# Kernel tuning notes

Hardware: AMD Instinct MI355X
Metric: run time of the kernel (lower is better)

Reference implementation:

```python
import jax, jax.numpy as jnp
import numpy as np

T, B, N = 5, 1048576, 16
GAMMA = 0.99


def setup_inputs() -> dict:
    key = jax.random.key(0)
    k = jax.random.split(key, 6)
    q = jax.random.normal(k[0], (B, N), dtype=jnp.float32)
    next_n_q = jax.random.normal(k[1], (B, N), dtype=jnp.float32)
    action = jax.random.randint(k[2], (B,), 0, N)
    next_n_action = jax.random.randint(k[3], (B,), 0, N)
    reward = jax.random.normal(k[4], (T, B), dtype=jnp.float32)
    done = jax.random.randint(k[5], (B,), 0, 2).astype(jnp.bool_)
    weight = jnp.ones((B,), dtype=jnp.float32)
    gamma = jnp.float32(GAMMA)
    return {"q": q, "next_n_q": next_n_q, "action": action,
            "next_n_action": next_n_action, "reward": reward,
            "done": done, "weight": weight, "gamma": gamma}


def reference(q, next_n_q, action, next_n_action, reward, done, weight, gamma):
    # q, next_n_q: (B, N); action/next_n_action/done/weight: (B,); reward: (T, B)
    t = reward.shape[0]
    # gather Q(s,a) and Q(s_{t+n}, a') by action index
    q_s_a = jnp.take_along_axis(q, action[:, None], axis=1)[:, 0]            # (B,)
    next_q_s_a = jnp.take_along_axis(next_n_q, next_n_action[:, None], axis=1)[:, 0]
    # n-step discounted return: sum_t gamma^t r_t + gamma^T * Q' * (1 - done)
    factors = gamma ** jnp.arange(t, dtype=q.dtype)                          # (T,)
    not_done = 1.0 - done.astype(q.dtype)
    target = jnp.einsum('t,tb->b', factors, reward) + (gamma ** t) * next_q_s_a * not_done
    target = jax.lax.stop_gradient(target)
    # per-sample MSE td error, weighted mean loss
    td_error_per_sample = jnp.square(q_s_a - target)                         # (B,)
    loss = jnp.mean(td_error_per_sample * weight)                            # ()
    return loss, td_error_per_sample
```

## Files before the change

kernel.cpp:

```cpp
#include <hip/hip_runtime.h>


__global__ __launch_bounds__(256) void qnstep_td_kernel(
    const float* __restrict__ q,
    const float* __restrict__ nq,
    const int*   __restrict__ act,
    const int*   __restrict__ nact,
    const float* __restrict__ rew,
    const int*   __restrict__ done,
    const float* __restrict__ w,
    const float* __restrict__ gamma_p,
    float*       __restrict__ out,
    int B, int N, int T, float invB)
{
    const int b = blockIdx.x * blockDim.x + threadIdx.x;
    const float gamma = gamma_p[0];

    float val = 0.0f;
    if (b < B) {
        float f = 1.0f, tgt = 0.0f;
        #pragma unroll 8
        for (int t = 0; t < T; ++t) {
            tgt += f * rew[t * B + b];
            f *= gamma;
        }
        const float nd  = (done[b] != 0) ? 0.0f : 1.0f;
        const float nqv = nq[(long long)b * N + nact[b]];
        tgt += f * nqv * nd;

        const float qa = q[(long long)b * N + act[b]];
        const float d  = qa - tgt;
        const float td = d * d;
        out[1 + b] = td;
        val = td * w[b];
    }

    #pragma unroll
    for (int off = 32; off > 0; off >>= 1)
        val += __shfl_down(val, off, 64);

    __shared__ float ssum[4];
    const int wave = threadIdx.x >> 6;
    const int lane = threadIdx.x & 63;
    if (lane == 0) ssum[wave] = val;
    __syncthreads();

    if (threadIdx.x == 0) {
        float s = ssum[0] + ssum[1] + ssum[2] + ssum[3];
        atomicAdd(out, s * invB);
    }
}

extern "C" void kernel_launch(void* const* d_in, const int* in_sizes, int n_in,
                              void* d_out, int out_size, void* d_ws, size_t ws_size,
                              hipStream_t stream) {
    const float* q     = (const float*)d_in[0];
    const float* nq    = (const float*)d_in[1];
    const int*   act   = (const int*)d_in[2];
    const int*   nact  = (const int*)d_in[3];
    const float* rew   = (const float*)d_in[4];
    const int*   done  = (const int*)d_in[5];
    const float* w     = (const float*)d_in[6];
    const float* gamma = (const float*)d_in[7];

    const int B = in_sizes[2];
    const int N = in_sizes[0] / B;
    const int T = in_sizes[4] / B;

    float* out = (float*)d_out;

    hipMemsetAsync(out, 0, sizeof(float), stream);

    const int block = 256;
    const int grid  = (B + block - 1) / block;
    qnstep_td_kernel<<<grid, block, 0, stream>>>(
        q, nq, act, nact, rew, done, w, gamma, out, B, N, T, 1.0f / (float)B);
}
```

Before: 200.5 us.

## Process four samples per thread with vector loads and two-pass reduction

Each thread now handles four consecutive samples, using int4/float4 loads for the action, done, weight and reward arrays. The per-block atomicAdd and the memset are replaced by per-block partials in workspace, which a single-block second kernel sums. This cuts the thread count, the number of load instructions and atomic contention, at the cost of an extra launch. The tail path for B not divisible by 4 is dropped, and the reduce kernel only covers up to 1024 partials, which holds for B=1M (1024 blocks).

```diff
diff --git a/kernel.cpp b/kernel.cpp
--- a/kernel.cpp
+++ b/kernel.cpp
@@ -1,7 +1,7 @@
 #include <hip/hip_runtime.h>
 
 
-__global__ __launch_bounds__(256) void qnstep_td_kernel(
+__global__ __launch_bounds__(256) void qnstep_td_main(
     const float* __restrict__ q,
     const float* __restrict__ nq,
     const int*   __restrict__ act,
@@ -11,28 +11,52 @@
     const float* __restrict__ w,
     const float* __restrict__ gamma_p,
     float*       __restrict__ out,
-    int B, int N, int T, float invB)
+    float*       __restrict__ partial,
+    int B, int N, int T)
 {
-    const int b = blockIdx.x * blockDim.x + threadIdx.x;
+    const int g  = blockIdx.x * blockDim.x + threadIdx.x;
+    const int b0 = g * 4;
     const float gamma = gamma_p[0];
 
     float val = 0.0f;
-    if (b < B) {
-        float f = 1.0f, tgt = 0.0f;
+    if (b0 + 3 < B) {
+        const int4   a4  = ((const int4*)act)[g];
+        const int4   na4 = ((const int4*)nact)[g];
+        const int4   d4  = ((const int4*)done)[g];
+        const float4 w4  = ((const float4*)w)[g];
+
+        float t0 = 0.f, t1 = 0.f, t2 = 0.f, t3 = 0.f;
+        float f = 1.0f;
         #pragma unroll 8
         for (int t = 0; t < T; ++t) {
-            tgt += f * rew[t * B + b];
+            const float4 r4 = ((const float4*)(rew + (long long)t * B))[g];
+            t0 += f * r4.x; t1 += f * r4.y; t2 += f * r4.z; t3 += f * r4.w;
             f *= gamma;
         }
-        const float nd  = (done[b] != 0) ? 0.0f : 1.0f;
-        const float nqv = nq[(long long)b * N + nact[b]];
-        tgt += f * nqv * nd;
 
-        const float qa = q[(long long)b * N + act[b]];
-        const float d  = qa - tgt;
-        const float td = d * d;
-        out[1 + b] = td;
-        val = td * w[b];
+        const float nq0 = nq[(long long)(b0 + 0) * N + na4.x];
+        const float nq1 = nq[(long long)(b0 + 1) * N + na4.y];
+        const float nq2 = nq[(long long)(b0 + 2) * N + na4.z];
+        const float nq3 = nq[(long long)(b0 + 3) * N + na4.w];
+        const float q0  = q [(long long)(b0 + 0) * N + a4.x];
+        const float q1  = q [(long long)(b0 + 1) * N + a4.y];
+        const float q2  = q [(long long)(b0 + 2) * N + a4.z];
+        const float q3  = q [(long long)(b0 + 3) * N + a4.w];
+
+        t0 += f * nq0 * (d4.x ? 0.f : 1.f);
+        t1 += f * nq1 * (d4.y ? 0.f : 1.f);
+        t2 += f * nq2 * (d4.z ? 0.f : 1.f);
+        t3 += f * nq3 * (d4.w ? 0.f : 1.f);
+
+        const float e0 = q0 - t0, e1 = q1 - t1, e2 = q2 - t2, e3 = q3 - t3;
+        const float td0 = e0 * e0, td1 = e1 * e1, td2 = e2 * e2, td3 = e3 * e3;
+
+        out[1 + b0 + 0] = td0;
+        out[1 + b0 + 1] = td1;
+        out[1 + b0 + 2] = td2;
+        out[1 + b0 + 3] = td3;
+
+        val = td0 * w4.x + td1 * w4.y + td2 * w4.z + td3 * w4.w;
     }
 
     #pragma unroll
@@ -45,9 +69,30 @@
     if (lane == 0) ssum[wave] = val;
     __syncthreads();
 
-    if (threadIdx.x == 0) {
-        float s = ssum[0] + ssum[1] + ssum[2] + ssum[3];
-        atomicAdd(out, s * invB);
+    if (threadIdx.x == 0)
+        partial[blockIdx.x] = ssum[0] + ssum[1] + ssum[2] + ssum[3];
+}
+
+__global__ __launch_bounds__(1024) void qnstep_td_reduce(
+    const float* __restrict__ partial, float* __restrict__ out,
+    int n, float invB)
+{
+    const int tid = threadIdx.x;
+    float v = (tid < n) ? partial[tid] : 0.0f;
+
+    #pragma unroll
+    for (int off = 32; off > 0; off >>= 1)
+        v += __shfl_down(v, off, 64);
+
+    __shared__ float ssum[16];
+    if ((tid & 63) == 0) ssum[tid >> 6] = v;
+    __syncthreads();
+
+    if (tid == 0) {
+        float s = 0.0f;
+        #pragma unroll
+        for (int i = 0; i < 16; ++i) s += ssum[i];
+        out[0] = s * invB;
     }
 }
 
@@ -67,12 +112,14 @@
     const int N = in_sizes[0] / B;
     const int T = in_sizes[4] / B;
 
-    float* out = (float*)d_out;
-
-    hipMemsetAsync(out, 0, sizeof(float), stream);
+    float* out     = (float*)d_out;
+    float* partial = (float*)d_ws;
 
     const int block = 256;
-    const int grid  = (B + block - 1) / block;
-    qnstep_td_kernel<<<grid, block, 0, stream>>>(
-        q, nq, act, nact, rew, done, w, gamma, out, B, N, T, 1.0f / (float)B);
+    const int gridA = (B + block * 4 - 1) / (block * 4);
+
+    qnstep_td_main<<<gridA, block, 0, stream>>>(
+        q, nq, act, nact, rew, done, w, gamma, out, partial, B, N, T);
+    qnstep_td_reduce<<<1, 1024, 0, stream>>>(
+        partial, out, gridA, 1.0f / (float)B);
 }
```

Measured after the change: 188.3 us. -6.1%, faster.

## Stage Q rows through LDS with coalesced loads and two-pass reduction

Applied to the files above, without the earlier changes.

For N=16, each block loads 512 full rows of q and next_n_q with coalesced float4 loads into shared memory and gathers the action values from there. Each thread processes two samples, using vectorized loads for actions, done flags, weights and rewards. The global atomicAdd and memset are replaced with per-block partial sums and a separate single-block reduce kernel. This trades an extra launch and more LDS use for better memory coalescing, with a generic fallback path kept for other shapes.

```diff
diff --git a/kernel.cpp b/kernel.cpp
--- a/kernel.cpp
+++ b/kernel.cpp
@@ -1,7 +1,10 @@
 #include <hip/hip_runtime.h>
 
 
-__global__ __launch_bounds__(256) void qnstep_td_kernel(
+#define TILE_ROWS 512
+#define BLOCK     256
+
+__global__ __launch_bounds__(BLOCK) void qnstep_td_main(
     const float* __restrict__ q,
     const float* __restrict__ nq,
     const int*   __restrict__ act,
@@ -11,43 +14,130 @@
     const float* __restrict__ w,
     const float* __restrict__ gamma_p,
     float*       __restrict__ out,
-    int B, int N, int T, float invB)
+    float*       __restrict__ partial,
+    int B, int T)
 {
-    const int b = blockIdx.x * blockDim.x + threadIdx.x;
+    __shared__ float tile[TILE_ROWS * 16];
+
+    const int tid  = threadIdx.x;
+    const long long base = (long long)blockIdx.x * TILE_ROWS;
     const float gamma = gamma_p[0];
 
-    float val = 0.0f;
-    if (b < B) {
-        float f = 1.0f, tgt = 0.0f;
-        #pragma unroll 8
-        for (int t = 0; t < T; ++t) {
-            tgt += f * rew[t * B + b];
-            f *= gamma;
-        }
-        const float nd  = (done[b] != 0) ? 0.0f : 1.0f;
-        const float nqv = nq[(long long)b * N + nact[b]];
-        tgt += f * nqv * nd;
+    const long long g = base / 2 + tid;
+    const int2   a2  = ((const int2*)act)[g];
+    const int2   na2 = ((const int2*)nact)[g];
+    const int2   d2  = ((const int2*)done)[g];
+    const float2 w2  = ((const float2*)w)[g];
 
-        const float qa = q[(long long)b * N + act[b]];
-        const float d  = qa - tgt;
-        const float td = d * d;
-        out[1 + b] = td;
-        val = td * w[b];
+    float t0 = 0.f, t1 = 0.f, f = 1.0f;
+    #pragma unroll 8
+    for (int t = 0; t < T; ++t) {
+        const float2 r2 = ((const float2*)(rew + (long long)t * B))[g];
+        t0 += f * r2.x; t1 += f * r2.y;
+        f *= gamma;
     }
+
+    const int s0 = tid * 2, s1 = tid * 2 + 1;
+
+    float4* t4 = (float4*)tile;
+    {
+        const float4* q4 = (const float4*)q + base * 4;
+        #pragma unroll
+        for (int j = 0; j < 8; ++j)
+            t4[tid + j * BLOCK] = q4[tid + j * BLOCK];
+    }
+    __syncthreads();
+    const float qa0 = tile[s0 * 16 + a2.x];
+    const float qa1 = tile[s1 * 16 + a2.y];
+    __syncthreads();
+
+    {
+        const float4* nq4 = (const float4*)nq + base * 4;
+        #pragma unroll
+        for (int j = 0; j < 8; ++j)
+            t4[tid + j * BLOCK] = nq4[tid + j * BLOCK];
+    }
+    __syncthreads();
+    const float nqa0 = tile[s0 * 16 + na2.x];
+    const float nqa1 = tile[s1 * 16 + na2.y];
+
+    t0 += f * nqa0 * (d2.x ? 0.f : 1.f);
+    t1 += f * nqa1 * (d2.y ? 0.f : 1.f);
+    const float e0 = qa0 - t0, e1 = qa1 - t1;
+    const float td0 = e0 * e0, td1 = e1 * e1;
+
+    out[1 + base + s0] = td0;
+    out[1 + base + s1] = td1;
+
+    float val = td0 * w2.x + td1 * w2.y;
 
     #pragma unroll
     for (int off = 32; off > 0; off >>= 1)
         val += __shfl_down(val, off, 64);
 
-    __shared__ float ssum[4];
-    const int wave = threadIdx.x >> 6;
-    const int lane = threadIdx.x & 63;
+    __shared__ float ssum[BLOCK / 64];
+    const int wave = tid >> 6, lane = tid & 63;
     if (lane == 0) ssum[wave] = val;
     __syncthreads();
+    if (tid == 0) {
+        float s = 0.f;
+        #pragma unroll
+        for (int i = 0; i < BLOCK / 64; ++i) s += ssum[i];
+        partial[blockIdx.x] = s;
+    }
+}
 
-    if (threadIdx.x == 0) {
-        float s = ssum[0] + ssum[1] + ssum[2] + ssum[3];
-        atomicAdd(out, s * invB);
+__global__ __launch_bounds__(256) void qnstep_td_generic(
+    const float* __restrict__ q, const float* __restrict__ nq,
+    const int* __restrict__ act, const int* __restrict__ nact,
+    const float* __restrict__ rew, const int* __restrict__ done,
+    const float* __restrict__ w, const float* __restrict__ gamma_p,
+    float* __restrict__ out, float* __restrict__ partial,
+    int B, int N, int T)
+{
+    const int b = blockIdx.x * blockDim.x + threadIdx.x;
+    const float gamma = gamma_p[0];
+    float val = 0.0f;
+    if (b < B) {
+        float f = 1.0f, tgt = 0.0f;
+        for (int t = 0; t < T; ++t) { tgt += f * rew[(long long)t * B + b]; f *= gamma; }
+        const float nd = (done[b] != 0) ? 0.f : 1.f;
+        tgt += f * nq[(long long)b * N + nact[b]] * nd;
+        const float d = q[(long long)b * N + act[b]] - tgt;
+        const float td = d * d;
+        out[1 + b] = td;
+        val = td * w[b];
+    }
+    #pragma unroll
+    for (int off = 32; off > 0; off >>= 1) val += __shfl_down(val, off, 64);
+    __shared__ float ssum[4];
+    if ((threadIdx.x & 63) == 0) ssum[threadIdx.x >> 6] = val;
+    __syncthreads();
+    if (threadIdx.x == 0)
+        partial[blockIdx.x] = ssum[0] + ssum[1] + ssum[2] + ssum[3];
+}
+
+__global__ __launch_bounds__(1024) void qnstep_td_reduce(
+    const float* __restrict__ partial, float* __restrict__ out,
+    int n, float invB)
+{
+    const int tid = threadIdx.x;
+    float v = 0.0f;
+    for (int i = tid; i < n; i += 1024) v += partial[i];
+
+    #pragma unroll
+    for (int off = 32; off > 0; off >>= 1)
+        v += __shfl_down(v, off, 64);
+
+    __shared__ float ssum[16];
+    if ((tid & 63) == 0) ssum[tid >> 6] = v;
+    __syncthreads();
+
+    if (tid == 0) {
+        float s = 0.0f;
+        #pragma unroll
+        for (int i = 0; i < 16; ++i) s += ssum[i];
+        out[0] = s * invB;
     }
 }
 
@@ -67,12 +157,18 @@
     const int N = in_sizes[0] / B;
     const int T = in_sizes[4] / B;
 
-    float* out = (float*)d_out;
+    float* out     = (float*)d_out;
+    float* partial = (float*)d_ws;
 
-    hipMemsetAsync(out, 0, sizeof(float), stream);
-
-    const int block = 256;
-    const int grid  = (B + block - 1) / block;
-    qnstep_td_kernel<<<grid, block, 0, stream>>>(
-        q, nq, act, nact, rew, done, w, gamma, out, B, N, T, 1.0f / (float)B);
+    if (N == 16 && (B % TILE_ROWS) == 0) {
+        const int grid = B / TILE_ROWS;
+        qnstep_td_main<<<grid, BLOCK, 0, stream>>>(
+            q, nq, act, nact, rew, done, w, gamma, out, partial, B, T);
+        qnstep_td_reduce<<<1, 1024, 0, stream>>>(partial, out, grid, 1.0f / (float)B);
+    } else {
+        const int grid = (B + 255) / 256;
+        qnstep_td_generic<<<grid, 256, 0, stream>>>(
+            q, nq, act, nact, rew, done, w, gamma, out, partial, B, N, T);
+        qnstep_td_reduce<<<1, 1024, 0, stream>>>(partial, out, grid, 1.0f / (float)B);
+    }
 }
```

After: 185.2 us. -7.6%, faster.

## Add persistent software-pipelined kernel with vectorized loads for N=16, T=5

Applied to the files above, without the earlier changes.

Adds a persistent grid-stride kernel (512 blocks) in which each thread handles two samples per iteration, using int2/float2 loads for the per-sample arrays and float4 loads for the gathered Q values. Index and reward loads are prefetched two iterations ahead and the dependent Q gathers one iteration ahead, so the gather latency overlaps with computation. The discount sum is unrolled as a Horner polynomial with a precomputed gamma^5. This path is specialised to N=16 and T=5, falls back to the generic kernel otherwise, and uses more registers for the pipeline.

```diff
diff --git a/kernel.cpp b/kernel.cpp
--- a/kernel.cpp
+++ b/kernel.cpp
@@ -1,7 +1,57 @@
 #include <hip/hip_runtime.h>
 
 
-__global__ __launch_bounds__(256) void qnstep_td_kernel(
+#define BLOCK 256
+#define GRID  512
+
+struct SStage {
+    int2   a, na, d;
+    float2 w;
+    float2 r0, r1, r2, r3, r4;
+};
+struct GStage {
+    float4 q0, q1, n0, n1;
+};
+
+__device__ __forceinline__ SStage load_s(
+    int g, const int* __restrict__ act, const int* __restrict__ nact,
+    const int* __restrict__ done, const float* __restrict__ w,
+    const float* __restrict__ rew, int PB)
+{
+    SStage s;
+    s.a  = ((const int2*)act)[g];
+    s.na = ((const int2*)nact)[g];
+    s.d  = ((const int2*)done)[g];
+    s.w  = ((const float2*)w)[g];
+    const float2* r = (const float2*)rew;
+    s.r0 = r[g];
+    s.r1 = r[g + PB];
+    s.r2 = r[g + 2 * PB];
+    s.r3 = r[g + 3 * PB];
+    s.r4 = r[g + 4 * PB];
+    return s;
+}
+
+__device__ __forceinline__ GStage load_g(
+    const SStage& s, int g, const float* __restrict__ q,
+    const float* __restrict__ nq)
+{
+    GStage o;
+    const long long b0 = (long long)g * 2;
+    o.q0 = *(const float4*)(q  + (b0 << 4)       + ((s.a.x  >> 2) << 2));
+    o.q1 = *(const float4*)(q  + ((b0 + 1) << 4) + ((s.a.y  >> 2) << 2));
+    o.n0 = *(const float4*)(nq + (b0 << 4)       + ((s.na.x >> 2) << 2));
+    o.n1 = *(const float4*)(nq + ((b0 + 1) << 4) + ((s.na.y >> 2) << 2));
+    return o;
+}
+
+__device__ __forceinline__ float sel4(const float4& v, int c) {
+    const float lo = (c & 1) ? v.y : v.x;
+    const float hi = (c & 1) ? v.w : v.z;
+    return (c & 2) ? hi : lo;
+}
+
+__global__ __launch_bounds__(BLOCK, 2) void qnstep_persist(
     const float* __restrict__ q,
     const float* __restrict__ nq,
     const int*   __restrict__ act,
@@ -11,44 +61,89 @@
     const float* __restrict__ w,
     const float* __restrict__ gamma_p,
     float*       __restrict__ out,
-    int B, int N, int T, float invB)
+    int B, int iters, float invB)
 {
-    const int b = blockIdx.x * blockDim.x + threadIdx.x;
+    const int stride = GRID * BLOCK;
+    const int PB = B >> 1;
+    int g = blockIdx.x * BLOCK + threadIdx.x;
     const float gamma = gamma_p[0];
+    const float g5 = gamma * gamma * gamma * gamma * gamma;
+
+    SStage s0  = load_s(g, act, nact, done, w, rew, PB);
+    SStage s1  = load_s(g + stride, act, nact, done, w, rew, PB);
+    GStage gg0 = load_g(s0, g, q, nq);
 
     float val = 0.0f;
-    if (b < B) {
-        float f = 1.0f, tgt = 0.0f;
-        #pragma unroll 8
-        for (int t = 0; t < T; ++t) {
-            tgt += f * rew[t * B + b];
-            f *= gamma;
-        }
-        const float nd  = (done[b] != 0) ? 0.0f : 1.0f;
-        const float nqv = nq[(long long)b * N + nact[b]];
-        tgt += f * nqv * nd;
+    for (int i = 0; i < iters; ++i) {
+        SStage s2  = {};
+        GStage gg1 = {};
+        if (i + 2 < iters) s2  = load_s(g + 2 * stride, act, nact, done, w, rew, PB);
+        if (i + 1 < iters) gg1 = load_g(s1, g + stride, q, nq);
 
-        const float qa = q[(long long)b * N + act[b]];
-        const float d  = qa - tgt;
-        const float td = d * d;
-        out[1 + b] = td;
-        val = td * w[b];
+        const long long b0 = (long long)g * 2;
+        float t0 = s0.r0.x + gamma * (s0.r1.x + gamma * (s0.r2.x + gamma * (s0.r3.x + gamma * s0.r4.x)));
+        float t1 = s0.r0.y + gamma * (s0.r1.y + gamma * (s0.r2.y + gamma * (s0.r3.y + gamma * s0.r4.y)));
+
+        const float qa0  = sel4(gg0.q0, s0.a.x  & 3);
+        const float qa1  = sel4(gg0.q1, s0.a.y  & 3);
+        const float nqa0 = sel4(gg0.n0, s0.na.x & 3);
+        const float nqa1 = sel4(gg0.n1, s0.na.y & 3);
+
+        t0 += g5 * nqa0 * (s0.d.x ? 0.f : 1.f);
+        t1 += g5 * nqa1 * (s0.d.y ? 0.f : 1.f);
+
+        const float e0 = qa0 - t0, e1 = qa1 - t1;
+        const float td0 = e0 * e0, td1 = e1 * e1;
+        out[1 + b0]     = td0;
+        out[2 + b0]     = td1;
+        val += td0 * s0.w.x + td1 * s0.w.y;
+
+        s0 = s1; s1 = s2; gg0 = gg1;
+        g += stride;
     }
 
     #pragma unroll
     for (int off = 32; off > 0; off >>= 1)
         val += __shfl_down(val, off, 64);
 
-    __shared__ float ssum[4];
-    const int wave = threadIdx.x >> 6;
-    const int lane = threadIdx.x & 63;
-    if (lane == 0) ssum[wave] = val;
+    __shared__ float ssum[BLOCK / 64];
+    if ((threadIdx.x & 63) == 0) ssum[threadIdx.x >> 6] = val;
     __syncthreads();
-
     if (threadIdx.x == 0) {
-        float s = ssum[0] + ssum[1] + ssum[2] + ssum[3];
+        float s = 0.f;
+        #pragma unroll
+        for (int i = 0; i < BLOCK / 64; ++i) s += ssum[i];
         atomicAdd(out, s * invB);
     }
+}
+
+__global__ __launch_bounds__(256) void qnstep_td_generic(
+    const float* __restrict__ q, const float* __restrict__ nq,
+    const int* __restrict__ act, const int* __restrict__ nact,
+    const float* __restrict__ rew, const int* __restrict__ done,
+    const float* __restrict__ w, const float* __restrict__ gamma_p,
+    float* __restrict__ out, int B, int N, int T, float invB)
+{
+    const int b = blockIdx.x * blockDim.x + threadIdx.x;
+    const float gamma = gamma_p[0];
+    float val = 0.0f;
+    if (b < B) {
+        float f = 1.0f, tgt = 0.0f;
+        for (int t = 0; t < T; ++t) { tgt += f * rew[(long long)t * B + b]; f *= gamma; }
+        const float nd = (done[b] != 0) ? 0.f : 1.f;
+        tgt += f * nq[(long long)b * N + nact[b]] * nd;
+        const float d = q[(long long)b * N + act[b]] - tgt;
+        const float td = d * d;
+        out[1 + b] = td;
+        val = td * w[b];
+    }
+    #pragma unroll
+    for (int off = 32; off > 0; off >>= 1) val += __shfl_down(val, off, 64);
+    __shared__ float ssum[4];
+    if ((threadIdx.x & 63) == 0) ssum[threadIdx.x >> 6] = val;
+    __syncthreads();
+    if (threadIdx.x == 0)
+        atomicAdd(out, (ssum[0] + ssum[1] + ssum[2] + ssum[3]) * invB);
 }
 
 extern "C" void kernel_launch(void* const* d_in, const int* in_sizes, int n_in,
@@ -71,8 +166,16 @@
 
     hipMemsetAsync(out, 0, sizeof(float), stream);
 
-    const int block = 256;
-    const int grid  = (B + block - 1) / block;
-    qnstep_td_kernel<<<grid, block, 0, stream>>>(
-        q, nq, act, nact, rew, done, w, gamma, out, B, N, T, 1.0f / (float)B);
+    const int chunk = GRID * BLOCK * 2;
+    const float invB = 1.0f / (float)B;
+
+    if (N == 16 && T == 5 && (B % chunk) == 0 && (B / chunk) >= 2) {
+        const int iters = B / chunk;
+        qnstep_persist<<<GRID, BLOCK, 0, stream>>>(
+            q, nq, act, nact, rew, done, w, gamma, out, B, iters, invB);
+    } else {
+        const int grid = (B + 255) / 256;
+        qnstep_td_generic<<<grid, 256, 0, stream>>>(
+            q, nq, act, nact, rew, done, w, gamma, out, B, N, T, invB);
+    }
 }
```

New measurement: 187.7 us. -6.4%, faster.
